# Optimization experiments

Hardware: AMD Instinct MI355X
Metric: run time of the kernel (lower is better)

Reference implementation:

```python
import jax, jax.numpy as jnp
import numpy as np

N, K, DC, DH = 50000, 32, 64, 64  # nodes, neighbors, dim_c(+dim_h), dim_hidden

def setup_inputs() -> dict:
    key = jax.random.key(0)
    ks = jax.random.split(key, 8)
    return {
        "z":     jax.random.normal(ks[0], (N, DC), dtype=jnp.float32),
        "z_":    jax.random.normal(ks[1], (N, K, DC), dtype=jnp.float32),
        "W_cur": jax.random.normal(ks[2], (DC, DH), dtype=jnp.float32) * 0.1,
        "b_cur": jax.random.uniform(ks[3], (DH,), minval=-0.1, maxval=0.1, dtype=jnp.float32),
        "W_nbr": jax.random.normal(ks[4], (2 * DC, DH), dtype=jnp.float32) * 0.1,
        "b_nbr": jax.random.uniform(ks[5], (DH,), minval=-0.1, maxval=0.1, dtype=jnp.float32),
        "W_out": jax.random.normal(ks[6], (2 * DH, DC), dtype=jnp.float32) * 0.1,
        "b_out": jax.random.uniform(ks[7], (DC,), minval=-0.1, maxval=0.1, dtype=jnp.float32),
    }

def reference(z, z_, W_cur, b_cur, W_nbr, b_nbr, W_out, b_out):
    # cur branch: CELU(Linear(z))  -> [N, DH]
    v = jax.nn.celu(z @ W_cur + b_cur)
    # nbr branch: concat(self expanded over nbr axis, neighbors) -> [N, K, 2*DC]
    zz = jnp.concatenate((jnp.broadcast_to(z[:, None, :], z_.shape), z_), axis=-1)
    # CELU(Linear) then sum over neighbor axis -> [N, DH]
    v_ = jax.nn.celu(zz @ W_nbr + b_nbr).sum(axis=-2)
    # final linear on concatenated features -> [N, DC]
    dc = jnp.concatenate((v, v_), axis=-1) @ W_out + b_out
    return dc
```

## Files before the change

kernel.cpp:

```cpp
#include <hip/hip_runtime.h>
#include <hip/hip_bf16.h>

typedef float  f32x16 __attribute__((ext_vector_type(16)));
typedef short  bf16x8 __attribute__((ext_vector_type(8)));

__device__ __forceinline__ unsigned short f2bf(float x) {
  union { float f; unsigned u; } v; v.f = x;
  return (unsigned short)((v.u + 0x7FFFu + ((v.u >> 16) & 1u)) >> 16);
}
__device__ __forceinline__ float bf2f(unsigned short u) {
  union { unsigned u; float f; } v; v.u = ((unsigned)u) << 16; return v.f;
}
__device__ __forceinline__ float celu1(float x) {
  return x > 0.f ? x : (__expf(x) - 1.f);
}

__device__ __forceinline__ bf16x8 to_frag(float4 a, float4 b) {
  bf16x8 r;
  r[0] = (short)f2bf(a.x); r[1] = (short)f2bf(a.y);
  r[2] = (short)f2bf(a.z); r[3] = (short)f2bf(a.w);
  r[4] = (short)f2bf(b.x); r[5] = (short)f2bf(b.y);
  r[6] = (short)f2bf(b.z); r[7] = (short)f2bf(b.w);
  return r;
}

__device__ __forceinline__ bf16x8 ldsfrag(const unsigned short* w, int S, int col, int k0) {
  return *reinterpret_cast<const bf16x8*>(w + col * S + (k0 ^ ((col & 7) << 3)));
}

__device__ __forceinline__ bf16x8 wfrag(const float* __restrict__ W, int ld, int col, int k0) {
  bf16x8 f;
#pragma unroll
  for (int j = 0; j < 8; ++j) f[j] = (short)f2bf(W[(size_t)(k0 + j) * ld + col]);
  return f;
}

__global__ __launch_bounds__(256, 2) void gcu_kernel(
    const float* __restrict__ z, const float* __restrict__ z_,
    const float* __restrict__ Wc, const float* __restrict__ bc,
    const float* __restrict__ Wn, const float* __restrict__ bn,
    const float* __restrict__ Wo, const float* __restrict__ bo,
    float* __restrict__ out, int N) {
  __shared__ __align__(16) unsigned short sWnT[64 * 128];
  __shared__ __align__(16) unsigned short sT[4][32 * 64];
  __shared__ __align__(16) unsigned short sV[4][32 * 64];
  __shared__ __align__(16) float sTile[4][32 * 64];

  const int tid = threadIdx.x;
  const int wid = tid >> 6, lane = tid & 63;
  const int lo = lane & 31, hi = lane >> 5;

  for (int i = tid; i < 128 * 64; i += 256) {
    int c = i & 63, k = i >> 6;
    sWnT[c * 128 + (k ^ ((c & 7) << 3))] = f2bf(Wn[i]);
  }
  __syncthreads();

  const int gw = blockIdx.x * 4 + wid;
  const int NW = (int)gridDim.x * 4;
  const int cnt = (N - gw + NW - 1) / NW;
  if (cnt <= 0) return;

  unsigned short* tt = &sT[wid][0];
  unsigned short* sv = &sV[wid][0];
  float* tile = &sTile[wid][0];

  const int rl = lane >> 4, tl = lane & 15;
  const int o0 = rl * 64 + ((tl ^ rl) << 2);
  const int o1 = o0 ^ 16;
  auto stage_tile = [&](const float* gb) {
#pragma unroll
    for (int i = 0; i < 8; ++i) {
      const float* src = gb + i * 256 + ((i & 1) ? o1 : o0);
      __builtin_amdgcn_global_load_lds(
          (const __attribute__((address_space(1))) unsigned*)src,
          (__attribute__((address_space(3))) unsigned*)(tile + i * 256),
          16, 0, 0);
    }
  };

  stage_tile(z_ + (size_t)gw * 2048);

  const float bn0 = bn[lo], bn1 = bn[32 + lo];
  const float bc0 = bc[lo], bc1 = bc[32 + lo];
  const float bo0 = bo[lo], bo1 = bo[32 + lo];

  bf16x8 zf[4];
  {
    int node = min(gw + lo * NW, N - 1);
    const float* zp = z + (size_t)node * 64;
#pragma unroll
    for (int ks = 0; ks < 4; ++ks) {
      float4 x0 = *reinterpret_cast<const float4*>(zp + ks * 16 + 8 * hi);
      float4 x1 = *reinterpret_cast<const float4*>(zp + ks * 16 + 8 * hi + 4);
      zf[ks] = to_frag(x0, x1);
    }
  }

  {
    f32x16 a0{}, a1{};
#pragma unroll
    for (int ks = 0; ks < 4; ++ks) {
      int k0 = ks * 16 + 8 * hi;
      bf16x8 b0 = ldsfrag(sWnT, 128, lo, k0);
      bf16x8 b1 = ldsfrag(sWnT, 128, lo + 32, k0);
      a0 = __builtin_amdgcn_mfma_f32_32x32x16_bf16(zf[ks], b0, a0, 0, 0, 0);
      a1 = __builtin_amdgcn_mfma_f32_32x32x16_bf16(zf[ks], b1, a1, 0, 0, 0);
    }
#pragma unroll
    for (int r = 0; r < 16; ++r) {
      int row = (r & 3) + 8 * (r >> 2) + 4 * hi;
      tt[row * 64 + lo]      = f2bf(a0[r]);
      tt[row * 64 + 32 + lo] = f2bf(a1[r]);
    }
  }

  bf16x8 Bn_[4][2];
#pragma unroll
  for (int ks = 0; ks < 4; ++ks) {
    int k0 = 64 + ks * 16 + 8 * hi;
    Bn_[ks][0] = ldsfrag(sWnT, 128, lo, k0);
    Bn_[ks][1] = ldsfrag(sWnT, 128, lo + 32, k0);
  }

  int roff[8];
#pragma unroll
  for (int ks = 0; ks < 4; ++ks)
#pragma unroll
    for (int p = 0; p < 2; ++p)
      roff[ks * 2 + p] = lo * 256 + (((ks * 4 + 2 * hi + p) ^ (lo & 7)) << 4);
  const char* tb = (const char*)tile;

#pragma unroll 1
  for (int nn = 0; nn < cnt; ++nn) {
    asm volatile("s_waitcnt vmcnt(0)" ::: "memory");
    __builtin_amdgcn_sched_barrier(0);
    float4 q[8];
#pragma unroll
    for (int j = 0; j < 8; ++j) q[j] = *reinterpret_cast<const float4*>(tb + roff[j]);
    bf16x8 af[4];
#pragma unroll
    for (int ks = 0; ks < 4; ++ks) af[ks] = to_frag(q[2 * ks], q[2 * ks + 1]);
    asm volatile("s_waitcnt lgkmcnt(0)" ::: "memory");
    __builtin_amdgcn_sched_barrier(0);
    if (nn + 1 < cnt) stage_tile(z_ + (size_t)(gw + (nn + 1) * NW) * 2048);

    float c0 = bn0 + bf2f(tt[nn * 64 + lo]);
    float c1 = bn1 + bf2f(tt[nn * 64 + 32 + lo]);
    f32x16 acc0{}, acc1{};
#pragma unroll
    for (int ks = 0; ks < 4; ++ks) {
      acc0 = __builtin_amdgcn_mfma_f32_32x32x16_bf16(af[ks], Bn_[ks][0], acc0, 0, 0, 0);
      acc1 = __builtin_amdgcn_mfma_f32_32x32x16_bf16(af[ks], Bn_[ks][1], acc1, 0, 0, 0);
    }
    float s0 = 0.f, s1 = 0.f;
#pragma unroll
    for (int r = 0; r < 16; ++r) {
      s0 += celu1(acc0[r] + c0);
      s1 += celu1(acc1[r] + c1);
    }
    s0 += __shfl_xor(s0, 32, 64);
    s1 += __shfl_xor(s1, 32, 64);
    if (hi == 0) {
      int m = (nn & 7) << 3;
      sv[nn * 64 + ( lo       ^ m)] = f2bf(s0);
      sv[nn * 64 + ((32 + lo) ^ m)] = f2bf(s1);
    }
  }

  unsigned short* vt = (unsigned short*)tile;
  asm volatile("s_waitcnt vmcnt(0)" ::: "memory");
  {
    f32x16 a0{}, a1{};
#pragma unroll
    for (int ks = 0; ks < 4; ++ks) {
      int k0 = ks * 16 + 8 * hi;
      a0 = __builtin_amdgcn_mfma_f32_32x32x16_bf16(zf[ks], wfrag(Wc, 64, lo, k0), a0, 0, 0, 0);
      a1 = __builtin_amdgcn_mfma_f32_32x32x16_bf16(zf[ks], wfrag(Wc, 64, lo + 32, k0), a1, 0, 0, 0);
    }
#pragma unroll
    for (int r = 0; r < 16; ++r) {
      int row = (r & 3) + 8 * (r >> 2) + 4 * hi;
      int m = (row & 7) << 3;
      vt[row * 64 + ( lo       ^ m)] = f2bf(celu1(a0[r] + bc0));
      vt[row * 64 + ((32 + lo) ^ m)] = f2bf(celu1(a1[r] + bc1));
    }
  }

  {
    f32x16 a0{}, a1{};
    const int mm = (lo & 7) << 3;
#pragma unroll
    for (int ks = 0; ks < 8; ++ks) {
      int k0 = ks * 16 + 8 * hi;
      bf16x8 af;
      if (ks < 4) af = *reinterpret_cast<const bf16x8*>(vt + lo * 64 + ( k0       ^ mm));
      else        af = *reinterpret_cast<const bf16x8*>(sv + lo * 64 + ((k0 - 64) ^ mm));
      a0 = __builtin_amdgcn_mfma_f32_32x32x16_bf16(af, wfrag(Wo, 64, lo, k0), a0, 0, 0, 0);
      a1 = __builtin_amdgcn_mfma_f32_32x32x16_bf16(af, wfrag(Wo, 64, lo + 32, k0), a1, 0, 0, 0);
    }
#pragma unroll
    for (int r = 0; r < 16; ++r) {
      int rr = (r & 3) + 8 * (r >> 2) + 4 * hi;
      int row = gw + rr * NW;
      if (row < N) {
        out[(size_t)row * 64 + lo]      = a0[r] + bo0;
        out[(size_t)row * 64 + 32 + lo] = a1[r] + bo1;
      }
    }
  }
}

extern "C" void kernel_launch(void* const* d_in, const int* in_sizes, int n_in,
                              void* d_out, int out_size, void* d_ws, size_t ws_size,
                              hipStream_t stream) {
  const float* z  = (const float*)d_in[0];
  const float* z_ = (const float*)d_in[1];
  const float* Wc = (const float*)d_in[2];
  const float* bc = (const float*)d_in[3];
  const float* Wn = (const float*)d_in[4];
  const float* bn = (const float*)d_in[5];
  const float* Wo = (const float*)d_in[6];
  const float* bo = (const float*)d_in[7];
  float* out = (float*)d_out;
  const int N = in_sizes[0] / 64;
  gcu_kernel<<<512, 256, 0, stream>>>(z, z_, Wc, bc, Wn, bn, Wo, bo, out, N);
}
```

Measured before the change: 87.50 us.

## Replace LDS tile staging with register double-buffered neighbor loads and raise occupancy

Drops the global_load_lds staging of each node's 32x64 neighbor tile into LDS and instead loads each lane's MFMA fragment straight into registers, with two stages in flight (ping-pong A/B). Float-to-bf16 conversion now uses a perm-based round-half-up pack instead of round-to-nearest-even. Removing the 32 KB tile buffer shrinks LDS use, so launch bounds go to 3 blocks per CU and the grid grows to 768 blocks. It also reuses the tt buffer for the final v tile. The register buffers add pressure under the tighter launch bound, and the rounding mode changes slightly.

```diff
diff --git a/kernel.cpp b/kernel.cpp
--- a/kernel.cpp
+++ b/kernel.cpp
@@ -24,6 +24,19 @@
   return r;
 }
 
+__device__ __forceinline__ unsigned pack_rh(unsigned ua, unsigned ub) {
+  return __builtin_amdgcn_perm(ub + 0x8000u, ua + 0x8000u, 0x07060302u);
+}
+__device__ __forceinline__ bf16x8 to_frag_rh(float4 a, float4 b) {
+  union { float4 f; unsigned u[4]; } A, B; A.f = a; B.f = b;
+  union { unsigned u[4]; bf16x8 v; } r;
+  r.u[0] = pack_rh(A.u[0], A.u[1]);
+  r.u[1] = pack_rh(A.u[2], A.u[3]);
+  r.u[2] = pack_rh(B.u[0], B.u[1]);
+  r.u[3] = pack_rh(B.u[2], B.u[3]);
+  return r.v;
+}
+
 __device__ __forceinline__ bf16x8 ldsfrag(const unsigned short* w, int S, int col, int k0) {
   return *reinterpret_cast<const bf16x8*>(w + col * S + (k0 ^ ((col & 7) << 3)));
 }
@@ -35,7 +48,9 @@
   return f;
 }
 
-__global__ __launch_bounds__(256, 2) void gcu_kernel(
+struct Stage { float4 a[4][2]; };
+
+__global__ __launch_bounds__(256, 3) void gcu_kernel(
     const float* __restrict__ z, const float* __restrict__ z_,
     const float* __restrict__ Wc, const float* __restrict__ bc,
     const float* __restrict__ Wn, const float* __restrict__ bn,
@@ -44,7 +59,6 @@
   __shared__ __align__(16) unsigned short sWnT[64 * 128];
   __shared__ __align__(16) unsigned short sT[4][32 * 64];
   __shared__ __align__(16) unsigned short sV[4][32 * 64];
-  __shared__ __align__(16) float sTile[4][32 * 64];
 
   const int tid = threadIdx.x;
   const int wid = tid >> 6, lane = tid & 63;
@@ -63,23 +77,16 @@
 
   unsigned short* tt = &sT[wid][0];
   unsigned short* sv = &sV[wid][0];
-  float* tile = &sTile[wid][0];
-
-  const int rl = lane >> 4, tl = lane & 15;
-  const int o0 = rl * 64 + ((tl ^ rl) << 2);
-  const int o1 = o0 ^ 16;
-  auto stage_tile = [&](const float* gb) {
-#pragma unroll
-    for (int i = 0; i < 8; ++i) {
-      const float* src = gb + i * 256 + ((i & 1) ? o1 : o0);
-      __builtin_amdgcn_global_load_lds(
-          (const __attribute__((address_space(1))) unsigned*)src,
-          (__attribute__((address_space(3))) unsigned*)(tile + i * 256),
-          16, 0, 0);
+
+  auto nodep = [&](int j) { return z_ + (size_t)min(gw + j * NW, N - 1) * 2048; };
+  auto issue_stage = [&](Stage& s, const float* p) {
+#pragma unroll
+    for (int ks = 0; ks < 4; ++ks) {
+      const float* pa = p + lo * 64 + ks * 16 + 8 * hi;
+      s.a[ks][0] = *reinterpret_cast<const float4*>(pa);
+      s.a[ks][1] = *reinterpret_cast<const float4*>(pa + 4);
     }
   };
-
-  stage_tile(z_ + (size_t)gw * 2048);
 
   const float bn0 = bn[lo], bn1 = bn[32 + lo];
   const float bc0 = bc[lo], bc1 = bc[32 + lo];
@@ -96,6 +103,10 @@
       zf[ks] = to_frag(x0, x1);
     }
   }
+
+  Stage sA, sB;
+  issue_stage(sA, nodep(0));
+  issue_stage(sB, nodep(1));
 
   {
     f32x16 a0{}, a1{};
@@ -123,36 +134,19 @@
     Bn_[ks][1] = ldsfrag(sWnT, 128, lo + 32, k0);
   }
 
-  int roff[8];
-#pragma unroll
-  for (int ks = 0; ks < 4; ++ks)
-#pragma unroll
-    for (int p = 0; p < 2; ++p)
-      roff[ks * 2 + p] = lo * 256 + (((ks * 4 + 2 * hi + p) ^ (lo & 7)) << 4);
-  const char* tb = (const char*)tile;
-
-#pragma unroll 1
-  for (int nn = 0; nn < cnt; ++nn) {
-    asm volatile("s_waitcnt vmcnt(0)" ::: "memory");
-    __builtin_amdgcn_sched_barrier(0);
-    float4 q[8];
-#pragma unroll
-    for (int j = 0; j < 8; ++j) q[j] = *reinterpret_cast<const float4*>(tb + roff[j]);
+  auto process = [&](Stage& s, int nn, const float* refill) {
     bf16x8 af[4];
 #pragma unroll
-    for (int ks = 0; ks < 4; ++ks) af[ks] = to_frag(q[2 * ks], q[2 * ks + 1]);
-    asm volatile("s_waitcnt lgkmcnt(0)" ::: "memory");
-    __builtin_amdgcn_sched_barrier(0);
-    if (nn + 1 < cnt) stage_tile(z_ + (size_t)(gw + (nn + 1) * NW) * 2048);
-
+    for (int ks = 0; ks < 4; ++ks) af[ks] = to_frag_rh(s.a[ks][0], s.a[ks][1]);
+    issue_stage(s, refill);
+    f32x16 acc0{}, acc1{};
+#pragma unroll
+    for (int ks = 0; ks < 4; ++ks) {
+      acc0 = __builtin_amdgcn_mfma_f32_32x32x16_bf16(af[ks], Bn_[ks][0], acc0, 0, 0, 0);
+      acc1 = __builtin_amdgcn_mfma_f32_32x32x16_bf16(af[ks], Bn_[ks][1], acc1, 0, 0, 0);
+    }
     float c0 = bn0 + bf2f(tt[nn * 64 + lo]);
     float c1 = bn1 + bf2f(tt[nn * 64 + 32 + lo]);
-    f32x16 acc0{}, acc1{};
-#pragma unroll
-    for (int ks = 0; ks < 4; ++ks) {
-      acc0 = __builtin_amdgcn_mfma_f32_32x32x16_bf16(af[ks], Bn_[ks][0], acc0, 0, 0, 0);
-      acc1 = __builtin_amdgcn_mfma_f32_32x32x16_bf16(af[ks], Bn_[ks][1], acc1, 0, 0, 0);
-    }
     float s0 = 0.f, s1 = 0.f;
 #pragma unroll
     for (int r = 0; r < 16; ++r) {
@@ -166,10 +160,17 @@
       sv[nn * 64 + ( lo       ^ m)] = f2bf(s0);
       sv[nn * 64 + ((32 + lo) ^ m)] = f2bf(s1);
     }
-  }
-
-  unsigned short* vt = (unsigned short*)tile;
-  asm volatile("s_waitcnt vmcnt(0)" ::: "memory");
+  };
+
+  const int pairs = cnt >> 1, odd = cnt & 1;
+#pragma unroll 1
+  for (int i = 0; i < pairs; ++i) {
+    process(sA, 2 * i,     nodep(2 * i + 2));
+    process(sB, 2 * i + 1, nodep(2 * i + 3));
+  }
+  if (odd) process(sA, cnt - 1, nodep(cnt - 1));
+
+  unsigned short* vt = tt;
   {
     f32x16 a0{}, a1{};
 #pragma unroll
@@ -224,5 +225,5 @@
   const float* bo = (const float*)d_in[7];
   float* out = (float*)d_out;
   const int N = in_sizes[0] / 64;
-  gcu_kernel<<<512, 256, 0, stream>>>(z, z_, Wc, bc, Wn, bn, Wo, bo, out, N);
-}
+  gcu_kernel<<<768, 256, 0, stream>>>(z, z_, Wc, bc, Wn, bn, Wo, bo, out, N);
+}
```

After: 103.5 us. 1.18x slower.
